# Kernel tuning notes

Measured on AMD Instinct MI355X. Metric: run time of the kernel, lower is better.

The kernel has to match this reference:

```python
import jax, jax.numpy as jnp
import numpy as np

N_NODES = 100000
N_EDGES = 1600000
NC = 32
N_MID = 8  # blocks 1..8 share structure [nc, nc//2, nc]


def setup_inputs() -> dict:
    key = jax.random.key(0)
    ks = jax.random.split(key, 12)
    x = jax.random.normal(ks[0], (N_NODES, 1), dtype=jnp.float32)
    edge_index = jax.random.randint(ks[1], (2, N_EDGES), 0, N_NODES, dtype=jnp.int32)
    s = 0.1
    # block 0: MLP [1, 16, 32]
    W1_0 = jax.random.normal(ks[2], (1, NC // 2), dtype=jnp.float32) * s
    b1_0 = jnp.zeros((NC // 2,), dtype=jnp.float32)
    W2_0 = jax.random.normal(ks[3], (NC // 2, NC), dtype=jnp.float32) * s
    b2_0 = jnp.zeros((NC,), dtype=jnp.float32)
    # blocks 1..8: MLP [32, 16, 32], stacked
    W1_mid = jax.random.normal(ks[4], (N_MID, NC, NC // 2), dtype=jnp.float32) * s
    b1_mid = jnp.zeros((N_MID, NC // 2), dtype=jnp.float32)
    W2_mid = jax.random.normal(ks[5], (N_MID, NC // 2, NC), dtype=jnp.float32) * s
    b2_mid = jnp.zeros((N_MID, NC), dtype=jnp.float32)
    # block 9: Linear(32, 1, bias=False)
    W_last = jax.random.normal(ks[6], (NC, 1), dtype=jnp.float32) * s
    return {
        "x": x, "edge_index": edge_index,
        "W1_0": W1_0, "b1_0": b1_0, "W2_0": W2_0, "b2_0": b2_0,
        "W1_mid": W1_mid, "b1_mid": b1_mid, "W2_mid": W2_mid, "b2_mid": b2_mid,
        "W_last": W_last,
    }


def _aggregate(h, src, dst):
    # GINConv sum aggregation: scatter-add messages x[src] into dst, eps=0.
    msg = h[src]  # [E, C]
    agg = jax.ops.segment_sum(msg, dst, num_segments=N_NODES)
    return h + agg  # (1+eps)*x + sum_j x_j, eps=0


def reference(x, edge_index, W1_0, b1_0, W2_0, b2_0,
              W1_mid, b1_mid, W2_mid, b2_mid, W_last):
    src = edge_index[0]
    dst = edge_index[1]
    # block 0: MLP([1,16,32]) -> Linear, SELU, (Dropout p=0 = id), Linear; no residual (1 != 32)
    h = _aggregate(x, src, dst)
    h = jax.nn.selu(h @ W1_0 + b1_0) @ W2_0 + b2_0
    # blocks 1..8: MLP([32,16,32]) with residual
    for i in range(N_MID):
        o = h
        h = _aggregate(h, src, dst)
        h = jax.nn.selu(h @ W1_mid[i] + b1_mid[i]) @ W2_mid[i] + b2_mid[i]
        h = h + o
    # block 9: Linear(32, 1, bias=False); no residual (32 != 1)
    h = _aggregate(h, src, dst)
    return h @ W_last
```

## Files before the change

### kernel.cpp

```cpp
#include <hip/hip_runtime.h>
#include <hip/hip_fp16.h>


typedef unsigned int uint_t;

#define NBLK 256
#define NBMAX 400

struct alignas(16) H2x4 { __half2 x, y, z, w; };

static __device__ __forceinline__ float selu_f(float x) {
    const float scale = 1.0507009873554805f;
    const float alpha = 1.6732632423543772f;
    return x > 0.f ? scale * x : scale * alpha * (__expf(x) - 1.f);
}

static __device__ __forceinline__ int pb0(int v) {
    return __builtin_amdgcn_mov_dpp(v, 0xA0, 0xf, 0xf, true);
}
static __device__ __forceinline__ int pb1(int v) {
    return __builtin_amdgcn_mov_dpp(v, 0xF5, 0xf, 0xf, true);
}
static __device__ __forceinline__ float pswap(float x) {
    return __int_as_float(__builtin_amdgcn_mov_dpp(__float_as_int(x), 0xB1, 0xf, 0xf, true));
}

static __device__ __forceinline__ void acc_add(__half2& a0, __half2& a1,
                                               __half2& a2, __half2& a3, H2x4 v) {
    a0 = __hadd2(a0, v.x); a1 = __hadd2(a1, v.y);
    a2 = __hadd2(a2, v.z); a3 = __hadd2(a3, v.w);
}


__global__ void k_hist(const int* __restrict__ dst, int* __restrict__ MT,
                       int e, int nb) {
    __shared__ int hist[NBMAX];
    for (int t = threadIdx.x; t < nb; t += 256) hist[t] = 0;
    __syncthreads();
    int chunk = (e + NBLK - 1) / NBLK;
    int lo = blockIdx.x * chunk, hi = min(e, lo + chunk);
    for (int i = lo + threadIdx.x; i < hi; i += 256)
        atomicAdd(&hist[dst[i] >> 8], 1);
    __syncthreads();
    for (int t = threadIdx.x; t < nb; t += 256)
        MT[t * NBLK + blockIdx.x] = hist[t];
}

__global__ void k_cscan(int* __restrict__ MT, int* __restrict__ tot, int nb) {
    int k = blockIdx.x;
    int lane = threadIdx.x;
    int carry = 0;
    #pragma unroll
    for (int r = 0; r < NBLK; r += 64) {
        int v = MT[k * NBLK + r + lane];
        int inc = v;
        #pragma unroll
        for (int d = 1; d < 64; d <<= 1) {
            int w = __shfl_up(inc, d, 64);
            if (lane >= d) inc += w;
        }
        MT[k * NBLK + r + lane] = carry + inc - v;
        carry += __shfl(inc, 63, 64);
    }
    if (lane == 0) tot[k] = carry;
}

__global__ void k_bscan(const int* __restrict__ tot, int* __restrict__ base,
                        int* __restrict__ rp, int nb, int e, int n) {
    __shared__ int s[512];
    int t = threadIdx.x;
    int v = (t < nb) ? tot[t] : 0;
    s[t] = v;
    __syncthreads();
    #pragma unroll
    for (int d = 1; d < 512; d <<= 1) {
        int w = (t >= d) ? s[t - d] : 0;
        __syncthreads();
        s[t] += w;
        __syncthreads();
    }
    if (t < nb) base[t] = s[t] - v;
    if (t == nb - 1) base[nb] = s[t];
    if (t == 0) rp[n] = e;
}

__global__ void k_scatter(const int* __restrict__ src, const int* __restrict__ dst,
                          const int* __restrict__ MT, const int* __restrict__ base,
                          uint_t* __restrict__ pairs, int e, int nb) {
    __shared__ int cur[NBMAX];
    for (int t = threadIdx.x; t < nb; t += 256)
        cur[t] = base[t] + MT[t * NBLK + blockIdx.x];
    __syncthreads();
    int chunk = (e + NBLK - 1) / NBLK;
    int lo = blockIdx.x * chunk, hi = min(e, lo + chunk);
    for (int i = lo + threadIdx.x; i < hi; i += 256) {
        int d = dst[i];
        int pos = atomicAdd(&cur[d >> 8], 1);
        pairs[pos] = (uint_t)src[i] | ((uint_t)(d & 255) << 24);
    }
}

__global__ void k_build(const uint_t* __restrict__ pairs, const int* __restrict__ base,
                        int* __restrict__ rp, int* __restrict__ esrc, int n) {
    int k = blockIdx.x;
    int bb = base[k], be = base[k + 1];
    __shared__ int cnt[256], cur[256], stmp[256];
    int t = threadIdx.x;
    cnt[t] = 0;
    __syncthreads();
    for (int i = bb + t; i < be; i += 256)
        atomicAdd(&cnt[pairs[i] >> 24], 1);
    __syncthreads();
    int v = cnt[t];
    stmp[t] = v;
    __syncthreads();
    #pragma unroll
    for (int d = 1; d < 256; d <<= 1) {
        int w = (t >= d) ? stmp[t - d] : 0;
        __syncthreads();
        stmp[t] += w;
        __syncthreads();
    }
    int excl = stmp[t] - v;
    int nd = k * 256 + t;
    if (nd < n) rp[nd] = bb + excl;
    cur[t] = bb + excl;
    __syncthreads();
    for (int i = bb + t; i < be; i += 256) {
        uint_t p = pairs[i];
        int pos = atomicAdd(&cur[p >> 24], 1);
        esrc[pos] = (int)(p & 0xFFFFFFu);
    }
}


__global__ void k_b0g(const float* __restrict__ x, const int* __restrict__ rp,
                      const int* __restrict__ esrc,
                      const float* __restrict__ W1, const float* __restrict__ b1,
                      const float* __restrict__ W2, const float* __restrict__ b2,
                      const float* __restrict__ W1next,
                      __half2* __restrict__ hout, __half2* __restrict__ gout, int n) {
    __shared__ float sW1[16], sb1[16], sW2[512], sb2[32], sWn[512];
    if (threadIdx.x < 16) { sW1[threadIdx.x] = W1[threadIdx.x]; sb1[threadIdx.x] = b1[threadIdx.x]; }
    for (int t = threadIdx.x; t < 512; t += 256) { sW2[t] = W2[t]; sWn[t] = W1next[t]; }
    if (threadIdx.x < 32) sb2[threadIdx.x] = b2[threadIdx.x];
    __syncthreads();
    int i = blockIdx.x * blockDim.x + threadIdx.x;
    if (i >= n) return;
    float a = x[i];
    int b = rp[i], en = rp[i + 1];
    int j = b;
    for (; j + 4 <= en; j += 4) {
        int s0 = esrc[j], s1 = esrc[j + 1], s2 = esrc[j + 2], s3 = esrc[j + 3];
        float x0 = x[s0], x1 = x[s1], x2 = x[s2], x3 = x[s3];
        a += (x0 + x1) + (x2 + x3);
    }
    for (; j < en; ++j) a += x[esrc[j]];
    float u[16];
    #pragma unroll
    for (int k = 0; k < 16; ++k) u[k] = selu_f(fmaf(a, sW1[k], sb1[k]));
    float row[32];
    #pragma unroll
    for (int jj = 0; jj < 32; ++jj) {
        float acc = sb2[jj];
        #pragma unroll
        for (int k = 0; k < 16; ++k) acc = fmaf(u[k], sW2[k * 32 + jj], acc);
        row[jj] = acc;
    }
    H2x4* op = (H2x4*)hout + (size_t)i * 4;
    #pragma unroll
    for (int q = 0; q < 4; ++q) {
        H2x4 vv;
        vv.x = __floats2half2_rn(row[q * 8 + 0], row[q * 8 + 1]);
        vv.y = __floats2half2_rn(row[q * 8 + 2], row[q * 8 + 3]);
        vv.z = __floats2half2_rn(row[q * 8 + 4], row[q * 8 + 5]);
        vv.w = __floats2half2_rn(row[q * 8 + 6], row[q * 8 + 7]);
        op[q] = vv;
    }
    float g[16];
    #pragma unroll
    for (int k = 0; k < 16; ++k) g[k] = 0.f;
    #pragma unroll
    for (int c = 0; c < 32; ++c) {
        float vc = row[c];
        #pragma unroll
        for (int k = 0; k < 16; ++k) g[k] = fmaf(vc, sWn[c * 16 + k], g[k]);
    }
    H2x4* gp = (H2x4*)gout + (size_t)i * 2;
    #pragma unroll
    for (int q = 0; q < 2; ++q) {
        H2x4 vv;
        vv.x = __floats2half2_rn(g[q * 8 + 0], g[q * 8 + 1]);
        vv.y = __floats2half2_rn(g[q * 8 + 2], g[q * 8 + 3]);
        vv.z = __floats2half2_rn(g[q * 8 + 4], g[q * 8 + 5]);
        vv.w = __floats2half2_rn(g[q * 8 + 6], g[q * 8 + 7]);
        gp[q] = vv;
    }
}

template<int MODE>
__global__ __launch_bounds__(256, 4) void k_gmid(
    const __half2* __restrict__ gin, const __half2* __restrict__ hin,
    const int* __restrict__ rp, const int* __restrict__ esrc,
    const float* __restrict__ W2, const float* __restrict__ b1,
    const float* __restrict__ b2, const float* __restrict__ Wnext,
    __half2* __restrict__ hout, __half2* __restrict__ gout,
    float* __restrict__ zout, int n) {
    __shared__ float sW2[512], sb1[16], sb2[32];
    __shared__ float sWn[512];
    for (int t = threadIdx.x; t < 512; t += 256) sW2[t] = W2[t];
    if (MODE == 0) {
        for (int t = threadIdx.x; t < 512; t += 256) sWn[t] = Wnext[t];
    } else {
        if (threadIdx.x < 32) sWn[threadIdx.x] = Wnext[threadIdx.x];
    }
    if (threadIdx.x < 16) sb1[threadIdx.x] = b1[threadIdx.x];
    else if (threadIdx.x < 48) sb2[threadIdx.x - 16] = b2[threadIdx.x - 16];
    __syncthreads();

    const int lane2 = threadIdx.x & 1;
    const int node = blockIdx.x * 128 + (threadIdx.x >> 1);
    if (node >= n) return;

    const H2x4* grows = (const H2x4*)gin;
    H2x4 a = grows[(size_t)node * 2 + lane2];
    __half2 a0 = a.x, a1 = a.y, a2 = a.z, a3 = a.w;

    int b = rp[node];
    int deg = rp[node + 1] - b;
    int j0 = 0;
    for (; j0 + 8 <= deg; j0 += 8) {
        int e0 = esrc[b + j0 + lane2];
        int e1 = esrc[b + j0 + 2 + lane2];
        int e2 = esrc[b + j0 + 4 + lane2];
        int e3 = esrc[b + j0 + 6 + lane2];
        int s0 = pb0(e0), s1 = pb1(e0), s2 = pb0(e1), s3 = pb1(e1);
        int s4 = pb0(e2), s5 = pb1(e2), s6 = pb0(e3), s7 = pb1(e3);
        H2x4 v0 = grows[(size_t)s0 * 2 + lane2];
        H2x4 v1 = grows[(size_t)s1 * 2 + lane2];
        H2x4 v2 = grows[(size_t)s2 * 2 + lane2];
        H2x4 v3 = grows[(size_t)s3 * 2 + lane2];
        H2x4 v4 = grows[(size_t)s4 * 2 + lane2];
        H2x4 v5 = grows[(size_t)s5 * 2 + lane2];
        H2x4 v6 = grows[(size_t)s6 * 2 + lane2];
        H2x4 v7 = grows[(size_t)s7 * 2 + lane2];
        acc_add(a0, a1, a2, a3, v0);
        acc_add(a0, a1, a2, a3, v1);
        acc_add(a0, a1, a2, a3, v2);
        acc_add(a0, a1, a2, a3, v3);
        acc_add(a0, a1, a2, a3, v4);
        acc_add(a0, a1, a2, a3, v5);
        acc_add(a0, a1, a2, a3, v6);
        acc_add(a0, a1, a2, a3, v7);
    }
    for (; j0 < deg; ++j0) {
        int s = esrc[b + j0];
        H2x4 v = grows[(size_t)s * 2 + lane2];
        acc_add(a0, a1, a2, a3, v);
    }

    float2 f0 = __half22float2(a0), f1 = __half22float2(a1),
           f2 = __half22float2(a2), f3 = __half22float2(a3);
    float u[8] = {f0.x, f0.y, f1.x, f1.y, f2.x, f2.y, f3.x, f3.y};
    const int kb = lane2 * 8;
    #pragma unroll
    for (int q = 0; q < 8; ++q) u[q] = selu_f(u[q] + sb1[kb + q]);

    float ua[16];
    #pragma unroll
    for (int q = 0; q < 8; ++q) {
        float uo = pswap(u[q]);
        ua[q]     = lane2 ? uo   : u[q];
        ua[8 + q] = lane2 ? u[q] : uo;
    }

    const H2x4* hrows = (const H2x4*)hin;
    H2x4 h0 = hrows[(size_t)node * 4 + lane2 * 2];
    H2x4 h1 = hrows[(size_t)node * 4 + lane2 * 2 + 1];
    float hv[16];
    {
        float2 g0 = __half22float2(h0.x), g1 = __half22float2(h0.y),
               g2 = __half22float2(h0.z), g3 = __half22float2(h0.w);
        float2 g4 = __half22float2(h1.x), g5 = __half22float2(h1.y),
               g6 = __half22float2(h1.z), g7 = __half22float2(h1.w);
        hv[0] = g0.x; hv[1] = g0.y; hv[2] = g1.x; hv[3] = g1.y;
        hv[4] = g2.x; hv[5] = g2.y; hv[6] = g3.x; hv[7] = g3.y;
        hv[8] = g4.x; hv[9] = g4.y; hv[10] = g5.x; hv[11] = g5.y;
        hv[12] = g6.x; hv[13] = g6.y; hv[14] = g7.x; hv[15] = g7.y;
    }

    const int jb = lane2 * 16;
    float o[16];
    #pragma unroll
    for (int q = 0; q < 16; ++q) {
        float oo = sb2[jb + q];
        #pragma unroll
        for (int k = 0; k < 16; ++k) oo = fmaf(ua[k], sW2[k * 32 + jb + q], oo);
        o[q] = oo + hv[q];
    }

    if (MODE == 0) {
        H2x4 o0, o1;
        o0.x = __floats2half2_rn(o[0], o[1]);   o0.y = __floats2half2_rn(o[2], o[3]);
        o0.z = __floats2half2_rn(o[4], o[5]);   o0.w = __floats2half2_rn(o[6], o[7]);
        o1.x = __floats2half2_rn(o[8], o[9]);   o1.y = __floats2half2_rn(o[10], o[11]);
        o1.z = __floats2half2_rn(o[12], o[13]); o1.w = __floats2half2_rn(o[14], o[15]);
        ((H2x4*)hout)[(size_t)node * 4 + lane2 * 2]     = o0;
        ((H2x4*)hout)[(size_t)node * 4 + lane2 * 2 + 1] = o1;
        float gp[16];
        #pragma unroll
        for (int k = 0; k < 16; ++k) gp[k] = 0.f;
        #pragma unroll
        for (int q = 0; q < 16; ++q) {
            float vc = o[q];
            #pragma unroll
            for (int k = 0; k < 16; ++k)
                gp[k] = fmaf(vc, sWn[(jb + q) * 16 + k], gp[k]);
        }
        #pragma unroll
        for (int k = 0; k < 16; ++k) gp[k] += pswap(gp[k]);
        H2x4 gv;
        gv.x = __floats2half2_rn(gp[kb + 0], gp[kb + 1]);
        gv.y = __floats2half2_rn(gp[kb + 2], gp[kb + 3]);
        gv.z = __floats2half2_rn(gp[kb + 4], gp[kb + 5]);
        gv.w = __floats2half2_rn(gp[kb + 6], gp[kb + 7]);
        ((H2x4*)gout)[(size_t)node * 2 + lane2] = gv;
    } else {
        float zp = 0.f;
        #pragma unroll
        for (int q = 0; q < 16; ++q) zp = fmaf(o[q], sWn[jb + q], zp);
        zp += pswap(zp);
        if (lane2 == 0) zout[node] = zp;
    }
}

__global__ void k_gz(const float* __restrict__ z, const int* __restrict__ rp,
                     const int* __restrict__ esrc, float* __restrict__ out, int n) {
    int i = blockIdx.x * blockDim.x + threadIdx.x;
    if (i >= n) return;
    float acc = z[i];
    int b = rp[i], en = rp[i + 1];
    int j = b;
    for (; j + 4 <= en; j += 4) {
        int s0 = esrc[j], s1 = esrc[j + 1], s2 = esrc[j + 2], s3 = esrc[j + 3];
        float z0 = z[s0], z1 = z[s1], z2 = z[s2], z3 = z[s3];
        acc += (z0 + z1) + (z2 + z3);
    }
    for (; j < en; ++j) acc += z[esrc[j]];
    out[i] = acc;
}


extern "C" void kernel_launch(void* const* d_in, const int* in_sizes, int n_in,
                              void* d_out, int out_size, void* d_ws, size_t ws_size,
                              hipStream_t stream) {
    const float* x    = (const float*)d_in[0];
    const int*   ei   = (const int*)d_in[1];
    const float* W1_0 = (const float*)d_in[2];
    const float* b1_0 = (const float*)d_in[3];
    const float* W2_0 = (const float*)d_in[4];
    const float* b2_0 = (const float*)d_in[5];
    const float* W1m  = (const float*)d_in[6];
    const float* b1m  = (const float*)d_in[7];
    const float* W2m  = (const float*)d_in[8];
    const float* b2m  = (const float*)d_in[9];
    const float* Wl   = (const float*)d_in[10];

    const int n = in_sizes[0];
    const int e = in_sizes[1] / 2;
    const int* src  = ei;
    const int* dstp = ei + e;
    const int nb = (n + 255) >> 8;

    char* ws = (char*)d_ws;
    size_t off = 0;
    auto alloc = [&](size_t bytes) -> char* {
        char* p = ws + off;
        off += (bytes + 255) & ~size_t(255);
        return p;
    };
    __half2* hP   = (__half2*)alloc((size_t)n * 32 * 2);
    __half2* hQ   = (__half2*)alloc((size_t)n * 32 * 2);
    __half2* gA   = (__half2*)alloc((size_t)n * 16 * 2);
    __half2* gB   = (__half2*)alloc((size_t)n * 16 * 2);
    float*   z    = (float*)alloc((size_t)n * 4);
    int*     rp   = (int*)alloc((size_t)(n + 1) * 4);
    int*     esrc = (int*)alloc((size_t)e * 4);
    uint_t*  pairs= (uint_t*)alloc((size_t)e * 4);
    int*     MT   = (int*)alloc((size_t)NBMAX * NBLK * 4);
    int*     base = (int*)alloc((size_t)(NBMAX + 1) * 4);
    int*     tot  = (int*)alloc((size_t)NBMAX * 4);
    (void)ws_size;

    const int B = 256;
    const int gN = (n + B - 1) / B;
    const int gG = (n + 127) / 128;

    k_hist<<<NBLK, B, 0, stream>>>(dstp, MT, e, nb);
    k_cscan<<<nb, 64, 0, stream>>>(MT, tot, nb);
    k_bscan<<<1, 512, 0, stream>>>(tot, base, rp, nb, e, n);
    k_scatter<<<NBLK, B, 0, stream>>>(src, dstp, MT, base, pairs, e, nb);
    k_build<<<nb, B, 0, stream>>>(pairs, base, rp, esrc, n);

    k_b0g<<<gN, B, 0, stream>>>(x, rp, esrc, W1_0, b1_0, W2_0, b2_0,
                                W1m , hP, gA, n);

    __half2* A = hP;  __half2* Bf = hQ;
    __half2* gin = gA; __half2* gnx = gB;
    for (int i = 0; i < 8; ++i) {
        if (i < 7) {
            k_gmid<0><<<gG, B, 0, stream>>>(gin, A, rp, esrc, W2m + i * 512,
                                            b1m + i * 16, b2m + i * 32,
                                            W1m + (i + 1) * 512,
                                            Bf, gnx, nullptr, n);
        } else {
            k_gmid<1><<<gG, B, 0, stream>>>(gin, A, rp, esrc, W2m + i * 512,
                                            b1m + i * 16, b2m + i * 32,
                                            Wl, Bf, nullptr, z, n);
        }
        __half2* t = A; A = Bf; Bf = t;
        __half2* tg = gin; gin = gnx; gnx = tg;
    }

    k_gz<<<gN, B, 0, stream>>>(z, rp, esrc, (float*)d_out, n);
}
```

Measured before the change: 267.7 us.

## Sort nodes by in-degree and process gather kernels in degree order

Builds a degree histogram during CSR construction, then scans it and scatters node ids into a permutation grouped by in-degree. All gather kernels (block 0, the mid blocks and the final z gather) now walk nodes through this permutation, so lanes in a wavefront have similar loop trip counts. This targets divergence from varied degrees, at the cost of two extra small kernels, a memset and one indirection per node, which makes the row reads and writes of hidden state non-contiguous. It also swaps size_t index arithmetic for 32-bit int arithmetic.

```diff
diff --git a/kernel.cpp b/kernel.cpp
--- a/kernel.cpp
+++ b/kernel.cpp
@@ -101,17 +101,21 @@
 }
 
 __global__ void k_build(const uint_t* __restrict__ pairs, const int* __restrict__ base,
-                        int* __restrict__ rp, int* __restrict__ esrc, int n) {
+                        int* __restrict__ rp, int* __restrict__ esrc,
+                        int* __restrict__ DH2, int n) {
     int k = blockIdx.x;
     int bb = base[k], be = base[k + 1];
-    __shared__ int cnt[256], cur[256], stmp[256];
+    __shared__ int cnt[256], cur[256], stmp[256], dh[64];
     int t = threadIdx.x;
     cnt[t] = 0;
+    if (t < 64) dh[t] = 0;
     __syncthreads();
     for (int i = bb + t; i < be; i += 256)
         atomicAdd(&cnt[pairs[i] >> 24], 1);
     __syncthreads();
     int v = cnt[t];
+    int nd = k * 256 + t;
+    if (nd < n) atomicAdd(&dh[min(v, 63)], 1);
     stmp[t] = v;
     __syncthreads();
     #pragma unroll
@@ -122,9 +126,9 @@
         __syncthreads();
     }
     int excl = stmp[t] - v;
-    int nd = k * 256 + t;
     if (nd < n) rp[nd] = bb + excl;
     cur[t] = bb + excl;
+    if (t < 64 && dh[t] > 0) atomicAdd(&DH2[t], dh[t]);
     __syncthreads();
     for (int i = bb + t; i < be; i += 256) {
         uint_t p = pairs[i];
@@ -133,9 +137,45 @@
     }
 }
 
+__global__ void k_dbase(const int* __restrict__ DH2, int* __restrict__ gcur) {
+    int lane = threadIdx.x;
+    int v = DH2[lane];
+    int inc = v;
+    #pragma unroll
+    for (int d = 1; d < 64; d <<= 1) {
+        int w = __shfl_up(inc, d, 64);
+        if (lane >= d) inc += w;
+    }
+    gcur[lane] = inc - v;
+}
+
+__global__ void k_dscatter(const int* __restrict__ rp, int* __restrict__ gcur,
+                           int* __restrict__ perm, int n) {
+    __shared__ int hist[64], bbase[64], cur2[64];
+    int t = threadIdx.x;
+    if (t < 64) hist[t] = 0;
+    __syncthreads();
+    int nd = blockIdx.x * 256 + t;
+    int bucket = 0;
+    if (nd < n) {
+        int deg = rp[nd + 1] - rp[nd];
+        bucket = min(deg, 63);
+        atomicAdd(&hist[bucket], 1);
+    }
+    __syncthreads();
+    if (t < 64 && hist[t] > 0) bbase[t] = atomicAdd(&gcur[t], hist[t]);
+    __syncthreads();
+    if (t < 64) cur2[t] = (hist[t] > 0) ? bbase[t] : 0;
+    __syncthreads();
+    if (nd < n) {
+        int pos = atomicAdd(&cur2[bucket], 1);
+        perm[pos] = nd;
+    }
+}
+
 
 __global__ void k_b0g(const float* __restrict__ x, const int* __restrict__ rp,
-                      const int* __restrict__ esrc,
+                      const int* __restrict__ esrc, const int* __restrict__ perm,
                       const float* __restrict__ W1, const float* __restrict__ b1,
                       const float* __restrict__ W2, const float* __restrict__ b2,
                       const float* __restrict__ W1next,
@@ -145,8 +185,9 @@
     for (int t = threadIdx.x; t < 512; t += 256) { sW2[t] = W2[t]; sWn[t] = W1next[t]; }
     if (threadIdx.x < 32) sb2[threadIdx.x] = b2[threadIdx.x];
     __syncthreads();
-    int i = blockIdx.x * blockDim.x + threadIdx.x;
-    if (i >= n) return;
+    int idx = blockIdx.x * blockDim.x + threadIdx.x;
+    if (idx >= n) return;
+    const int i = perm[idx];
     float a = x[i];
     int b = rp[i], en = rp[i + 1];
     int j = b;
@@ -167,7 +208,7 @@
         for (int k = 0; k < 16; ++k) acc = fmaf(u[k], sW2[k * 32 + jj], acc);
         row[jj] = acc;
     }
-    H2x4* op = (H2x4*)hout + (size_t)i * 4;
+    H2x4* op = (H2x4*)hout + i * 4;
     #pragma unroll
     for (int q = 0; q < 4; ++q) {
         H2x4 vv;
@@ -186,7 +227,7 @@
         #pragma unroll
         for (int k = 0; k < 16; ++k) g[k] = fmaf(vc, sWn[c * 16 + k], g[k]);
     }
-    H2x4* gp = (H2x4*)gout + (size_t)i * 2;
+    H2x4* gp = (H2x4*)gout + i * 2;
     #pragma unroll
     for (int q = 0; q < 2; ++q) {
         H2x4 vv;
@@ -202,6 +243,7 @@
 __global__ __launch_bounds__(256, 4) void k_gmid(
     const __half2* __restrict__ gin, const __half2* __restrict__ hin,
     const int* __restrict__ rp, const int* __restrict__ esrc,
+    const int* __restrict__ perm,
     const float* __restrict__ W2, const float* __restrict__ b1,
     const float* __restrict__ b2, const float* __restrict__ Wnext,
     __half2* __restrict__ hout, __half2* __restrict__ gout,
@@ -219,11 +261,12 @@
     __syncthreads();
 
     const int lane2 = threadIdx.x & 1;
-    const int node = blockIdx.x * 128 + (threadIdx.x >> 1);
-    if (node >= n) return;
+    const int idx = blockIdx.x * 128 + (threadIdx.x >> 1);
+    if (idx >= n) return;
+    const int node = perm[idx];
 
     const H2x4* grows = (const H2x4*)gin;
-    H2x4 a = grows[(size_t)node * 2 + lane2];
+    H2x4 a = grows[node * 2 + lane2];
     __half2 a0 = a.x, a1 = a.y, a2 = a.z, a3 = a.w;
 
     int b = rp[node];
@@ -236,14 +279,14 @@
         int e3 = esrc[b + j0 + 6 + lane2];
         int s0 = pb0(e0), s1 = pb1(e0), s2 = pb0(e1), s3 = pb1(e1);
         int s4 = pb0(e2), s5 = pb1(e2), s6 = pb0(e3), s7 = pb1(e3);
-        H2x4 v0 = grows[(size_t)s0 * 2 + lane2];
-        H2x4 v1 = grows[(size_t)s1 * 2 + lane2];
-        H2x4 v2 = grows[(size_t)s2 * 2 + lane2];
-        H2x4 v3 = grows[(size_t)s3 * 2 + lane2];
-        H2x4 v4 = grows[(size_t)s4 * 2 + lane2];
-        H2x4 v5 = grows[(size_t)s5 * 2 + lane2];
-        H2x4 v6 = grows[(size_t)s6 * 2 + lane2];
-        H2x4 v7 = grows[(size_t)s7 * 2 + lane2];
+        H2x4 v0 = grows[s0 * 2 + lane2];
+        H2x4 v1 = grows[s1 * 2 + lane2];
+        H2x4 v2 = grows[s2 * 2 + lane2];
+        H2x4 v3 = grows[s3 * 2 + lane2];
+        H2x4 v4 = grows[s4 * 2 + lane2];
+        H2x4 v5 = grows[s5 * 2 + lane2];
+        H2x4 v6 = grows[s6 * 2 + lane2];
+        H2x4 v7 = grows[s7 * 2 + lane2];
         acc_add(a0, a1, a2, a3, v0);
         acc_add(a0, a1, a2, a3, v1);
         acc_add(a0, a1, a2, a3, v2);
@@ -255,7 +298,7 @@
     }
     for (; j0 < deg; ++j0) {
         int s = esrc[b + j0];
-        H2x4 v = grows[(size_t)s * 2 + lane2];
+        H2x4 v = grows[s * 2 + lane2];
         acc_add(a0, a1, a2, a3, v);
     }
 
@@ -275,8 +318,8 @@
     }
 
     const H2x4* hrows = (const H2x4*)hin;
-    H2x4 h0 = hrows[(size_t)node * 4 + lane2 * 2];
-    H2x4 h1 = hrows[(size_t)node * 4 + lane2 * 2 + 1];
+    H2x4 h0 = hrows[node * 4 + lane2 * 2];
+    H2x4 h1 = hrows[node * 4 + lane2 * 2 + 1];
     float hv[16];
     {
         float2 g0 = __half22float2(h0.x), g1 = __half22float2(h0.y),
@@ -305,8 +348,8 @@
         o0.z = __floats2half2_rn(o[4], o[5]);   o0.w = __floats2half2_rn(o[6], o[7]);
         o1.x = __floats2half2_rn(o[8], o[9]);   o1.y = __floats2half2_rn(o[10], o[11]);
         o1.z = __floats2half2_rn(o[12], o[13]); o1.w = __floats2half2_rn(o[14], o[15]);
-        ((H2x4*)hout)[(size_t)node * 4 + lane2 * 2]     = o0;
-        ((H2x4*)hout)[(size_t)node * 4 + lane2 * 2 + 1] = o1;
+        ((H2x4*)hout)[node * 4 + lane2 * 2]     = o0;
+        ((H2x4*)hout)[node * 4 + lane2 * 2 + 1] = o1;
         float gp[16];
         #pragma unroll
         for (int k = 0; k < 16; ++k) gp[k] = 0.f;
@@ -324,7 +367,7 @@
         gv.y = __floats2half2_rn(gp[kb + 2], gp[kb + 3]);
         gv.z = __floats2half2_rn(gp[kb + 4], gp[kb + 5]);
         gv.w = __floats2half2_rn(gp[kb + 6], gp[kb + 7]);
-        ((H2x4*)gout)[(size_t)node * 2 + lane2] = gv;
+        ((H2x4*)gout)[node * 2 + lane2] = gv;
     } else {
         float zp = 0.f;
         #pragma unroll
@@ -335,9 +378,11 @@
 }
 
 __global__ void k_gz(const float* __restrict__ z, const int* __restrict__ rp,
-                     const int* __restrict__ esrc, float* __restrict__ out, int n) {
-    int i = blockIdx.x * blockDim.x + threadIdx.x;
-    if (i >= n) return;
+                     const int* __restrict__ esrc, const int* __restrict__ perm,
+                     float* __restrict__ out, int n) {
+    int idx = blockIdx.x * blockDim.x + threadIdx.x;
+    if (idx >= n) return;
+    const int i = perm[idx];
     float acc = z[i];
     int b = rp[i], en = rp[i + 1];
     int j = b;
@@ -390,37 +435,44 @@
     int*     MT   = (int*)alloc((size_t)NBMAX * NBLK * 4);
     int*     base = (int*)alloc((size_t)(NBMAX + 1) * 4);
     int*     tot  = (int*)alloc((size_t)NBMAX * 4);
+    int*     perm = (int*)alloc((size_t)n * 4);
+    int*     DH2  = (int*)alloc(64 * 4);
+    int*     gcur = (int*)alloc(64 * 4);
     (void)ws_size;
 
     const int B = 256;
     const int gN = (n + B - 1) / B;
     const int gG = (n + 127) / 128;
 
+    hipMemsetAsync(DH2, 0, 64 * 4, stream);
     k_hist<<<NBLK, B, 0, stream>>>(dstp, MT, e, nb);
     k_cscan<<<nb, 64, 0, stream>>>(MT, tot, nb);
     k_bscan<<<1, 512, 0, stream>>>(tot, base, rp, nb, e, n);
     k_scatter<<<NBLK, B, 0, stream>>>(src, dstp, MT, base, pairs, e, nb);
-    k_build<<<nb, B, 0, stream>>>(pairs, base, rp, esrc, n);
-
-    k_b0g<<<gN, B, 0, stream>>>(x, rp, esrc, W1_0, b1_0, W2_0, b2_0,
+    k_build<<<nb, B, 0, stream>>>(pairs, base, rp, esrc, DH2, n);
+    k_dbase<<<1, 64, 0, stream>>>(DH2, gcur);
+    k_dscatter<<<nb, B, 0, stream>>>(rp, gcur, perm, n);
+
+    k_b0g<<<gN, B, 0, stream>>>(x, rp, esrc, perm, W1_0, b1_0, W2_0, b2_0,
                                 W1m , hP, gA, n);
 
     __half2* A = hP;  __half2* Bf = hQ;
     __half2* gin = gA; __half2* gnx = gB;
     for (int i = 0; i < 8; ++i) {
         if (i < 7) {
-            k_gmid<0><<<gG, B, 0, stream>>>(gin, A, rp, esrc, W2m + i * 512,
-                                            b1m + i * 16, b2m + i * 32,
-                                            W1m + (i + 1) * 512,
+            k_gmid<0><<<gG, B, 0, stream>>>(gin, A, rp, esrc, perm,
+                                            W2m + i * 512, b1m + i * 16,
+                                            b2m + i * 32, W1m + (i + 1) * 512,
                                             Bf, gnx, nullptr, n);
         } else {
-            k_gmid<1><<<gG, B, 0, stream>>>(gin, A, rp, esrc, W2m + i * 512,
-                                            b1m + i * 16, b2m + i * 32,
-                                            Wl, Bf, nullptr, z, n);
+            k_gmid<1><<<gG, B, 0, stream>>>(gin, A, rp, esrc, perm,
+                                            W2m + i * 512, b1m + i * 16,
+                                            b2m + i * 32, Wl,
+                                            Bf, nullptr, z, n);
         }
         __half2* t = A; A = Bf; Bf = t;
         __half2* tg = gin; gin = gnx; gnx = tg;
     }
 
-    k_gz<<<gN, B, 0, stream>>>(z, rp, esrc, (float*)d_out, n);
-}
+    k_gz<<<gN, B, 0, stream>>>(z, rp, esrc, perm, (float*)d_out, n);
+}
```

Result: slower. 334.9 us (+25.1%).

## Use four lanes per node in gather-MLP kernels and two lanes in scalar gathers

Applied to the files above, without the earlier changes.

Each node in the middle GIN layers is now handled by four lanes instead of two. Two lane pairs gather alternate 8-edge chunks, padding with a zeroed dummy row at index n, and their sums are combined through DPP row swaps. The dense W2/Wnext products are split so each lane computes 8 output columns using float4 LDS reads. The first-layer kernel and the final scalar aggregation now split each node's edge list across two lanes. The aim is more memory-level parallelism and lower per-thread latency on the irregular gathers, at the cost of extra masked loads, cross-lane reductions and two small memsets.

```diff
diff --git a/kernel.cpp b/kernel.cpp
--- a/kernel.cpp
+++ b/kernel.cpp
@@ -8,6 +8,7 @@
 #define NBMAX 400
 
 struct alignas(16) H2x4 { __half2 x, y, z, w; };
+struct alignas(8)  H2x2 { __half2 x, y; };
 
 static __device__ __forceinline__ float selu_f(float x) {
     const float scale = 1.0507009873554805f;
@@ -23,6 +24,15 @@
 }
 static __device__ __forceinline__ float pswap(float x) {
     return __int_as_float(__builtin_amdgcn_mov_dpp(__float_as_int(x), 0xB1, 0xf, 0xf, true));
+}
+static __device__ __forceinline__ float qx2f(float x) {
+    return __int_as_float(__builtin_amdgcn_mov_dpp(__float_as_int(x), 0x4E, 0xf, 0xf, true));
+}
+static __device__ __forceinline__ __half2 h2qx2(__half2 v) {
+    int i; __builtin_memcpy(&i, &v, 4);
+    i = __builtin_amdgcn_mov_dpp(i, 0x4E, 0xf, 0xf, true);
+    __half2 r; __builtin_memcpy(&r, &i, 4);
+    return r;
 }
 
 static __device__ __forceinline__ void acc_add(__half2& a0, __half2& a1,
@@ -134,68 +144,100 @@
 }
 
 
-__global__ void k_b0g(const float* __restrict__ x, const int* __restrict__ rp,
-                      const int* __restrict__ esrc,
-                      const float* __restrict__ W1, const float* __restrict__ b1,
-                      const float* __restrict__ W2, const float* __restrict__ b2,
-                      const float* __restrict__ W1next,
-                      __half2* __restrict__ hout, __half2* __restrict__ gout, int n) {
-    __shared__ float sW1[16], sb1[16], sW2[512], sb2[32], sWn[512];
-    if (threadIdx.x < 16) { sW1[threadIdx.x] = W1[threadIdx.x]; sb1[threadIdx.x] = b1[threadIdx.x]; }
+__global__ __launch_bounds__(256) void k_b0g(
+    const float* __restrict__ x, const int* __restrict__ rp,
+    const int* __restrict__ esrc,
+    const float* __restrict__ W1, const float* __restrict__ b1,
+    const float* __restrict__ W2, const float* __restrict__ b2,
+    const float* __restrict__ W1next,
+    __half2* __restrict__ hout, __half2* __restrict__ gout, int n) {
+    __shared__ __align__(16) float sW1[16], sb1v[16], sW2[512], sb2v[32], sWn[512];
+    if (threadIdx.x < 16) { sW1[threadIdx.x] = W1[threadIdx.x]; sb1v[threadIdx.x] = b1[threadIdx.x]; }
     for (int t = threadIdx.x; t < 512; t += 256) { sW2[t] = W2[t]; sWn[t] = W1next[t]; }
-    if (threadIdx.x < 32) sb2[threadIdx.x] = b2[threadIdx.x];
-    __syncthreads();
-    int i = blockIdx.x * blockDim.x + threadIdx.x;
-    if (i >= n) return;
-    float a = x[i];
-    int b = rp[i], en = rp[i + 1];
-    int j = b;
-    for (; j + 4 <= en; j += 4) {
-        int s0 = esrc[j], s1 = esrc[j + 1], s2 = esrc[j + 2], s3 = esrc[j + 3];
-        float x0 = x[s0], x1 = x[s1], x2 = x[s2], x3 = x[s3];
-        a += (x0 + x1) + (x2 + x3);
-    }
-    for (; j < en; ++j) a += x[esrc[j]];
+    if (threadIdx.x < 32) sb2v[threadIdx.x] = b2[threadIdx.x];
+    __syncthreads();
+    const int lane2 = threadIdx.x & 1;
+    const int node = blockIdx.x * 128 + (threadIdx.x >> 1);
+    if (node >= n) return;
+
+    const int b = rp[node];
+    const int deg = rp[node + 1] - b;
+    const int half = deg >> 1;
+    const int lo = lane2 ? half : 0;
+    const int hi = lane2 ? deg : half;
+    float a = lane2 ? 0.f : x[node];
+    int j = lo;
+    for (; j + 4 <= hi; j += 4) {
+        int s0 = esrc[b + j], s1 = esrc[b + j + 1],
+            s2 = esrc[b + j + 2], s3 = esrc[b + j + 3];
+        float v0 = x[s0], v1 = x[s1], v2 = x[s2], v3 = x[s3];
+        a += (v0 + v1) + (v2 + v3);
+    }
+    for (; j < hi; ++j) a += x[esrc[b + j]];
+    a += pswap(a);
+
     float u[16];
     #pragma unroll
-    for (int k = 0; k < 16; ++k) u[k] = selu_f(fmaf(a, sW1[k], sb1[k]));
-    float row[32];
-    #pragma unroll
-    for (int jj = 0; jj < 32; ++jj) {
-        float acc = sb2[jj];
-        #pragma unroll
-        for (int k = 0; k < 16; ++k) acc = fmaf(u[k], sW2[k * 32 + jj], acc);
-        row[jj] = acc;
-    }
-    H2x4* op = (H2x4*)hout + (size_t)i * 4;
-    #pragma unroll
-    for (int q = 0; q < 4; ++q) {
-        H2x4 vv;
-        vv.x = __floats2half2_rn(row[q * 8 + 0], row[q * 8 + 1]);
-        vv.y = __floats2half2_rn(row[q * 8 + 2], row[q * 8 + 3]);
-        vv.z = __floats2half2_rn(row[q * 8 + 4], row[q * 8 + 5]);
-        vv.w = __floats2half2_rn(row[q * 8 + 6], row[q * 8 + 7]);
-        op[q] = vv;
-    }
-    float g[16];
-    #pragma unroll
-    for (int k = 0; k < 16; ++k) g[k] = 0.f;
-    #pragma unroll
-    for (int c = 0; c < 32; ++c) {
-        float vc = row[c];
-        #pragma unroll
-        for (int k = 0; k < 16; ++k) g[k] = fmaf(vc, sWn[c * 16 + k], g[k]);
-    }
-    H2x4* gp = (H2x4*)gout + (size_t)i * 2;
-    #pragma unroll
-    for (int q = 0; q < 2; ++q) {
-        H2x4 vv;
-        vv.x = __floats2half2_rn(g[q * 8 + 0], g[q * 8 + 1]);
-        vv.y = __floats2half2_rn(g[q * 8 + 2], g[q * 8 + 3]);
-        vv.z = __floats2half2_rn(g[q * 8 + 4], g[q * 8 + 5]);
-        vv.w = __floats2half2_rn(g[q * 8 + 6], g[q * 8 + 7]);
-        gp[q] = vv;
-    }
+    for (int k = 0; k < 16; ++k) u[k] = selu_f(fmaf(a, sW1[k], sb1v[k]));
+
+    const int jb = lane2 * 16;
+    float row[16];
+    #pragma unroll
+    for (int q = 0; q < 16; ++q) row[q] = sb2v[jb + q];
+    #pragma unroll
+    for (int k = 0; k < 16; ++k) {
+        const float4 w0 = *(const float4*)&sW2[k * 32 + jb];
+        const float4 w1 = *(const float4*)&sW2[k * 32 + jb + 4];
+        const float4 w2 = *(const float4*)&sW2[k * 32 + jb + 8];
+        const float4 w3 = *(const float4*)&sW2[k * 32 + jb + 12];
+        float uk = u[k];
+        row[0]  = fmaf(uk, w0.x, row[0]);  row[1]  = fmaf(uk, w0.y, row[1]);
+        row[2]  = fmaf(uk, w0.z, row[2]);  row[3]  = fmaf(uk, w0.w, row[3]);
+        row[4]  = fmaf(uk, w1.x, row[4]);  row[5]  = fmaf(uk, w1.y, row[5]);
+        row[6]  = fmaf(uk, w1.z, row[6]);  row[7]  = fmaf(uk, w1.w, row[7]);
+        row[8]  = fmaf(uk, w2.x, row[8]);  row[9]  = fmaf(uk, w2.y, row[9]);
+        row[10] = fmaf(uk, w2.z, row[10]); row[11] = fmaf(uk, w2.w, row[11]);
+        row[12] = fmaf(uk, w3.x, row[12]); row[13] = fmaf(uk, w3.y, row[13]);
+        row[14] = fmaf(uk, w3.z, row[14]); row[15] = fmaf(uk, w3.w, row[15]);
+    }
+    H2x4 o0, o1;
+    o0.x = __floats2half2_rn(row[0], row[1]);   o0.y = __floats2half2_rn(row[2], row[3]);
+    o0.z = __floats2half2_rn(row[4], row[5]);   o0.w = __floats2half2_rn(row[6], row[7]);
+    o1.x = __floats2half2_rn(row[8], row[9]);   o1.y = __floats2half2_rn(row[10], row[11]);
+    o1.z = __floats2half2_rn(row[12], row[13]); o1.w = __floats2half2_rn(row[14], row[15]);
+    ((H2x4*)hout)[node * 4 + lane2 * 2]     = o0;
+    ((H2x4*)hout)[node * 4 + lane2 * 2 + 1] = o1;
+
+    float gp[16];
+    #pragma unroll
+    for (int k = 0; k < 16; ++k) gp[k] = 0.f;
+    #pragma unroll
+    for (int q = 0; q < 16; ++q) {
+        const float4 w0 = *(const float4*)&sWn[(jb + q) * 16];
+        const float4 w1 = *(const float4*)&sWn[(jb + q) * 16 + 4];
+        const float4 w2 = *(const float4*)&sWn[(jb + q) * 16 + 8];
+        const float4 w3 = *(const float4*)&sWn[(jb + q) * 16 + 12];
+        float vq = row[q];
+        gp[0]  = fmaf(vq, w0.x, gp[0]);  gp[1]  = fmaf(vq, w0.y, gp[1]);
+        gp[2]  = fmaf(vq, w0.z, gp[2]);  gp[3]  = fmaf(vq, w0.w, gp[3]);
+        gp[4]  = fmaf(vq, w1.x, gp[4]);  gp[5]  = fmaf(vq, w1.y, gp[5]);
+        gp[6]  = fmaf(vq, w1.z, gp[6]);  gp[7]  = fmaf(vq, w1.w, gp[7]);
+        gp[8]  = fmaf(vq, w2.x, gp[8]);  gp[9]  = fmaf(vq, w2.y, gp[9]);
+        gp[10] = fmaf(vq, w2.z, gp[10]); gp[11] = fmaf(vq, w2.w, gp[11]);
+        gp[12] = fmaf(vq, w3.x, gp[12]); gp[13] = fmaf(vq, w3.y, gp[13]);
+        gp[14] = fmaf(vq, w3.z, gp[14]); gp[15] = fmaf(vq, w3.w, gp[15]);
+    }
+    float r[8];
+    #pragma unroll
+    for (int i = 0; i < 8; ++i) {
+        float lo_ = gp[i]     + pswap(gp[i]);
+        float hi_ = gp[8 + i] + pswap(gp[8 + i]);
+        r[i] = lane2 ? hi_ : lo_;
+    }
+    H2x4 gv;
+    gv.x = __floats2half2_rn(r[0], r[1]); gv.y = __floats2half2_rn(r[2], r[3]);
+    gv.z = __floats2half2_rn(r[4], r[5]); gv.w = __floats2half2_rn(r[6], r[7]);
+    ((H2x4*)gout)[node * 2 + lane2] = gv;
 }
 
 template<int MODE>
@@ -206,8 +248,7 @@
     const float* __restrict__ b2, const float* __restrict__ Wnext,
     __half2* __restrict__ hout, __half2* __restrict__ gout,
     float* __restrict__ zout, int n) {
-    __shared__ float sW2[512], sb1[16], sb2[32];
-    __shared__ float sWn[512];
+    __shared__ __align__(16) float sW2[512], sb1[16], sb2[32], sWn[512];
     for (int t = threadIdx.x; t < 512; t += 256) sW2[t] = W2[t];
     if (MODE == 0) {
         for (int t = threadIdx.x; t < 512; t += 256) sWn[t] = Wnext[t];
@@ -218,32 +259,42 @@
     else if (threadIdx.x < 48) sb2[threadIdx.x - 16] = b2[threadIdx.x - 16];
     __syncthreads();
 
-    const int lane2 = threadIdx.x & 1;
-    const int node = blockIdx.x * 128 + (threadIdx.x >> 1);
+    const int lane4 = threadIdx.x & 3;
+    const int c = lane4 & 1;
+    const int p = lane4 >> 1;
+    const int node = blockIdx.x * 64 + (threadIdx.x >> 2);
     if (node >= n) return;
 
     const H2x4* grows = (const H2x4*)gin;
-    H2x4 a = grows[(size_t)node * 2 + lane2];
-    __half2 a0 = a.x, a1 = a.y, a2 = a.z, a3 = a.w;
-
-    int b = rp[node];
-    int deg = rp[node + 1] - b;
-    int j0 = 0;
-    for (; j0 + 8 <= deg; j0 += 8) {
-        int e0 = esrc[b + j0 + lane2];
-        int e1 = esrc[b + j0 + 2 + lane2];
-        int e2 = esrc[b + j0 + 4 + lane2];
-        int e3 = esrc[b + j0 + 6 + lane2];
+    H2x4 self = grows[node * 2 + c];
+    __half2 hzero = __floats2half2_rn(0.f, 0.f);
+    __half2 a0 = p ? hzero : self.x, a1 = p ? hzero : self.y,
+            a2 = p ? hzero : self.z, a3 = p ? hzero : self.w;
+
+    const int b = rp[node];
+    const int deg = rp[node + 1] - b;
+    const int ZR = n;
+    for (int j0 = 0; j0 < deg; j0 += 16) {
+        int lo = j0 + 8 * p;
+        int m = deg - lo; m = m < 0 ? 0 : (m > 8 ? 8 : m);
+        int i0 = lo + c,     i1 = lo + 2 + c, i2 = lo + 4 + c, i3 = lo + 6 + c;
+        i0 = i0 < deg ? i0 : 0; i1 = i1 < deg ? i1 : 0;
+        i2 = i2 < deg ? i2 : 0; i3 = i3 < deg ? i3 : 0;
+        int e0 = esrc[b + i0], e1 = esrc[b + i1], e2 = esrc[b + i2], e3 = esrc[b + i3];
         int s0 = pb0(e0), s1 = pb1(e0), s2 = pb0(e1), s3 = pb1(e1);
         int s4 = pb0(e2), s5 = pb1(e2), s6 = pb0(e3), s7 = pb1(e3);
-        H2x4 v0 = grows[(size_t)s0 * 2 + lane2];
-        H2x4 v1 = grows[(size_t)s1 * 2 + lane2];
-        H2x4 v2 = grows[(size_t)s2 * 2 + lane2];
-        H2x4 v3 = grows[(size_t)s3 * 2 + lane2];
-        H2x4 v4 = grows[(size_t)s4 * 2 + lane2];
-        H2x4 v5 = grows[(size_t)s5 * 2 + lane2];
-        H2x4 v6 = grows[(size_t)s6 * 2 + lane2];
-        H2x4 v7 = grows[(size_t)s7 * 2 + lane2];
+        s0 = 0 < m ? s0 : ZR; s1 = 1 < m ? s1 : ZR;
+        s2 = 2 < m ? s2 : ZR; s3 = 3 < m ? s3 : ZR;
+        s4 = 4 < m ? s4 : ZR; s5 = 5 < m ? s5 : ZR;
+        s6 = 6 < m ? s6 : ZR; s7 = 7 < m ? s7 : ZR;
+        H2x4 v0 = grows[s0 * 2 + c];
+        H2x4 v1 = grows[s1 * 2 + c];
+        H2x4 v2 = grows[s2 * 2 + c];
+        H2x4 v3 = grows[s3 * 2 + c];
+        H2x4 v4 = grows[s4 * 2 + c];
+        H2x4 v5 = grows[s5 * 2 + c];
+        H2x4 v6 = grows[s6 * 2 + c];
+        H2x4 v7 = grows[s7 * 2 + c];
         acc_add(a0, a1, a2, a3, v0);
         acc_add(a0, a1, a2, a3, v1);
         acc_add(a0, a1, a2, a3, v2);
@@ -253,16 +304,13 @@
         acc_add(a0, a1, a2, a3, v6);
         acc_add(a0, a1, a2, a3, v7);
     }
-    for (; j0 < deg; ++j0) {
-        int s = esrc[b + j0];
-        H2x4 v = grows[(size_t)s * 2 + lane2];
-        acc_add(a0, a1, a2, a3, v);
-    }
+    a0 = __hadd2(a0, h2qx2(a0)); a1 = __hadd2(a1, h2qx2(a1));
+    a2 = __hadd2(a2, h2qx2(a2)); a3 = __hadd2(a3, h2qx2(a3));
 
     float2 f0 = __half22float2(a0), f1 = __half22float2(a1),
            f2 = __half22float2(a2), f3 = __half22float2(a3);
     float u[8] = {f0.x, f0.y, f1.x, f1.y, f2.x, f2.y, f3.x, f3.y};
-    const int kb = lane2 * 8;
+    const int kb = c * 8;
     #pragma unroll
     for (int q = 0; q < 8; ++q) u[q] = selu_f(u[q] + sb1[kb + q]);
 
@@ -270,84 +318,103 @@
     #pragma unroll
     for (int q = 0; q < 8; ++q) {
         float uo = pswap(u[q]);
-        ua[q]     = lane2 ? uo   : u[q];
-        ua[8 + q] = lane2 ? u[q] : uo;
-    }
-
+        ua[q]     = c ? uo   : u[q];
+        ua[8 + q] = c ? u[q] : uo;
+    }
+
+    const int jb = lane4 * 8;
     const H2x4* hrows = (const H2x4*)hin;
-    H2x4 h0 = hrows[(size_t)node * 4 + lane2 * 2];
-    H2x4 h1 = hrows[(size_t)node * 4 + lane2 * 2 + 1];
-    float hv[16];
-    {
-        float2 g0 = __half22float2(h0.x), g1 = __half22float2(h0.y),
-               g2 = __half22float2(h0.z), g3 = __half22float2(h0.w);
-        float2 g4 = __half22float2(h1.x), g5 = __half22float2(h1.y),
-               g6 = __half22float2(h1.z), g7 = __half22float2(h1.w);
-        hv[0] = g0.x; hv[1] = g0.y; hv[2] = g1.x; hv[3] = g1.y;
-        hv[4] = g2.x; hv[5] = g2.y; hv[6] = g3.x; hv[7] = g3.y;
-        hv[8] = g4.x; hv[9] = g4.y; hv[10] = g5.x; hv[11] = g5.y;
-        hv[12] = g6.x; hv[13] = g6.y; hv[14] = g7.x; hv[15] = g7.y;
-    }
-
-    const int jb = lane2 * 16;
-    float o[16];
-    #pragma unroll
-    for (int q = 0; q < 16; ++q) {
-        float oo = sb2[jb + q];
-        #pragma unroll
-        for (int k = 0; k < 16; ++k) oo = fmaf(ua[k], sW2[k * 32 + jb + q], oo);
-        o[q] = oo + hv[q];
+    H2x4 h0 = hrows[node * 4 + lane4];
+    float2 g0 = __half22float2(h0.x), g1 = __half22float2(h0.y),
+           g2 = __half22float2(h0.z), g3 = __half22float2(h0.w);
+    float o[8] = {g0.x, g0.y, g1.x, g1.y, g2.x, g2.y, g3.x, g3.y};
+    #pragma unroll
+    for (int q = 0; q < 8; ++q) o[q] += sb2[jb + q];
+    #pragma unroll
+    for (int k = 0; k < 16; ++k) {
+        const float4 w0 = *(const float4*)&sW2[k * 32 + jb];
+        const float4 w1 = *(const float4*)&sW2[k * 32 + jb + 4];
+        float uk = ua[k];
+        o[0] = fmaf(uk, w0.x, o[0]); o[1] = fmaf(uk, w0.y, o[1]);
+        o[2] = fmaf(uk, w0.z, o[2]); o[3] = fmaf(uk, w0.w, o[3]);
+        o[4] = fmaf(uk, w1.x, o[4]); o[5] = fmaf(uk, w1.y, o[5]);
+        o[6] = fmaf(uk, w1.z, o[6]); o[7] = fmaf(uk, w1.w, o[7]);
     }
 
     if (MODE == 0) {
-        H2x4 o0, o1;
-        o0.x = __floats2half2_rn(o[0], o[1]);   o0.y = __floats2half2_rn(o[2], o[3]);
-        o0.z = __floats2half2_rn(o[4], o[5]);   o0.w = __floats2half2_rn(o[6], o[7]);
-        o1.x = __floats2half2_rn(o[8], o[9]);   o1.y = __floats2half2_rn(o[10], o[11]);
-        o1.z = __floats2half2_rn(o[12], o[13]); o1.w = __floats2half2_rn(o[14], o[15]);
-        ((H2x4*)hout)[(size_t)node * 4 + lane2 * 2]     = o0;
-        ((H2x4*)hout)[(size_t)node * 4 + lane2 * 2 + 1] = o1;
+        H2x4 ov;
+        ov.x = __floats2half2_rn(o[0], o[1]); ov.y = __floats2half2_rn(o[2], o[3]);
+        ov.z = __floats2half2_rn(o[4], o[5]); ov.w = __floats2half2_rn(o[6], o[7]);
+        ((H2x4*)hout)[node * 4 + lane4] = ov;
+
         float gp[16];
         #pragma unroll
         for (int k = 0; k < 16; ++k) gp[k] = 0.f;
         #pragma unroll
-        for (int q = 0; q < 16; ++q) {
-            float vc = o[q];
-            #pragma unroll
-            for (int k = 0; k < 16; ++k)
-                gp[k] = fmaf(vc, sWn[(jb + q) * 16 + k], gp[k]);
+        for (int q = 0; q < 8; ++q) {
+            const float4 w0 = *(const float4*)&sWn[(jb + q) * 16];
+            const float4 w1 = *(const float4*)&sWn[(jb + q) * 16 + 4];
+            const float4 w2 = *(const float4*)&sWn[(jb + q) * 16 + 8];
+            const float4 w3 = *(const float4*)&sWn[(jb + q) * 16 + 12];
+            float vq = o[q];
+            gp[0]  = fmaf(vq, w0.x, gp[0]);  gp[1]  = fmaf(vq, w0.y, gp[1]);
+            gp[2]  = fmaf(vq, w0.z, gp[2]);  gp[3]  = fmaf(vq, w0.w, gp[3]);
+            gp[4]  = fmaf(vq, w1.x, gp[4]);  gp[5]  = fmaf(vq, w1.y, gp[5]);
+            gp[6]  = fmaf(vq, w1.z, gp[6]);  gp[7]  = fmaf(vq, w1.w, gp[7]);
+            gp[8]  = fmaf(vq, w2.x, gp[8]);  gp[9]  = fmaf(vq, w2.y, gp[9]);
+            gp[10] = fmaf(vq, w2.z, gp[10]); gp[11] = fmaf(vq, w2.w, gp[11]);
+            gp[12] = fmaf(vq, w3.x, gp[12]); gp[13] = fmaf(vq, w3.y, gp[13]);
+            gp[14] = fmaf(vq, w3.z, gp[14]); gp[15] = fmaf(vq, w3.w, gp[15]);
         }
-        #pragma unroll
-        for (int k = 0; k < 16; ++k) gp[k] += pswap(gp[k]);
-        H2x4 gv;
-        gv.x = __floats2half2_rn(gp[kb + 0], gp[kb + 1]);
-        gv.y = __floats2half2_rn(gp[kb + 2], gp[kb + 3]);
-        gv.z = __floats2half2_rn(gp[kb + 4], gp[kb + 5]);
-        gv.w = __floats2half2_rn(gp[kb + 6], gp[kb + 7]);
-        ((H2x4*)gout)[(size_t)node * 2 + lane2] = gv;
+        float r[8];
+        #pragma unroll
+        for (int i = 0; i < 8; ++i) {
+            float lo_ = gp[i]     + pswap(gp[i]);
+            float hi_ = gp[8 + i] + pswap(gp[8 + i]);
+            r[i] = c ? hi_ : lo_;
+        }
+        float rr[4];
+        #pragma unroll
+        for (int i = 0; i < 4; ++i) {
+            float lo_ = r[i]     + qx2f(r[i]);
+            float hi_ = r[4 + i] + qx2f(r[4 + i]);
+            rr[i] = p ? hi_ : lo_;
+        }
+        H2x2 gv;
+        gv.x = __floats2half2_rn(rr[0], rr[1]);
+        gv.y = __floats2half2_rn(rr[2], rr[3]);
+        ((H2x2*)gout)[node * 4 + c * 2 + p] = gv;
     } else {
         float zp = 0.f;
         #pragma unroll
-        for (int q = 0; q < 16; ++q) zp = fmaf(o[q], sWn[jb + q], zp);
+        for (int q = 0; q < 8; ++q) zp = fmaf(o[q], sWn[jb + q], zp);
         zp += pswap(zp);
-        if (lane2 == 0) zout[node] = zp;
+        zp += qx2f(zp);
+        if (lane4 == 0) zout[node] = zp;
     }
 }
 
 __global__ void k_gz(const float* __restrict__ z, const int* __restrict__ rp,
                      const int* __restrict__ esrc, float* __restrict__ out, int n) {
-    int i = blockIdx.x * blockDim.x + threadIdx.x;
-    if (i >= n) return;
-    float acc = z[i];
-    int b = rp[i], en = rp[i + 1];
-    int j = b;
-    for (; j + 4 <= en; j += 4) {
-        int s0 = esrc[j], s1 = esrc[j + 1], s2 = esrc[j + 2], s3 = esrc[j + 3];
+    const int lane2 = threadIdx.x & 1;
+    const int node = blockIdx.x * 128 + (threadIdx.x >> 1);
+    if (node >= n) return;
+    const int b = rp[node];
+    const int deg = rp[node + 1] - b;
+    const int half = deg >> 1;
+    const int lo = lane2 ? half : 0;
+    const int hi = lane2 ? deg : half;
+    float acc = lane2 ? 0.f : z[node];
+    int j = lo;
+    for (; j + 4 <= hi; j += 4) {
+        int s0 = esrc[b + j], s1 = esrc[b + j + 1],
+            s2 = esrc[b + j + 2], s3 = esrc[b + j + 3];
         float z0 = z[s0], z1 = z[s1], z2 = z[s2], z3 = z[s3];
         acc += (z0 + z1) + (z2 + z3);
     }
-    for (; j < en; ++j) acc += z[esrc[j]];
-    out[i] = acc;
+    for (; j < hi; ++j) acc += z[esrc[b + j]];
+    acc += pswap(acc);
+    if (lane2 == 0) out[node] = acc;
 }
 
 
@@ -368,7 +435,7 @@
 
     const int n = in_sizes[0];
     const int e = in_sizes[1] / 2;
-    const int* src  = ei;
+    const int* srcp = ei;
     const int* dstp = ei + e;
     const int nb = (n + 255) >> 8;
 
@@ -381,8 +448,8 @@
     };
     __half2* hP   = (__half2*)alloc((size_t)n * 32 * 2);
     __half2* hQ   = (__half2*)alloc((size_t)n * 32 * 2);
-    __half2* gA   = (__half2*)alloc((size_t)n * 16 * 2);
-    __half2* gB   = (__half2*)alloc((size_t)n * 16 * 2);
+    __half2* gA   = (__half2*)alloc((size_t)(n + 1) * 16 * 2);
+    __half2* gB   = (__half2*)alloc((size_t)(n + 1) * 16 * 2);
     float*   z    = (float*)alloc((size_t)n * 4);
     int*     rp   = (int*)alloc((size_t)(n + 1) * 4);
     int*     esrc = (int*)alloc((size_t)e * 4);
@@ -394,33 +461,38 @@
 
     const int B = 256;
     const int gN = (n + B - 1) / B;
-    const int gG = (n + 127) / 128;
+    const int g2 = (n + 127) / 128;
+    const int g4 = (n + 63) / 64;
+
+    hipMemsetAsync(gA + (size_t)n * 8, 0, 32, stream);
+    hipMemsetAsync(gB + (size_t)n * 8, 0, 32, stream);
 
     k_hist<<<NBLK, B, 0, stream>>>(dstp, MT, e, nb);
     k_cscan<<<nb, 64, 0, stream>>>(MT, tot, nb);
     k_bscan<<<1, 512, 0, stream>>>(tot, base, rp, nb, e, n);
-    k_scatter<<<NBLK, B, 0, stream>>>(src, dstp, MT, base, pairs, e, nb);
+    k_scatter<<<NBLK, B, 0, stream>>>(srcp, dstp, MT, base, pairs, e, nb);
     k_build<<<nb, B, 0, stream>>>(pairs, base, rp, esrc, n);
 
-    k_b0g<<<gN, B, 0, stream>>>(x, rp, esrc, W1_0, b1_0, W2_0, b2_0,
+    k_b0g<<<g2, B, 0, stream>>>(x, rp, esrc, W1_0, b1_0, W2_0, b2_0,
                                 W1m , hP, gA, n);
 
     __half2* A = hP;  __half2* Bf = hQ;
     __half2* gin = gA; __half2* gnx = gB;
     for (int i = 0; i < 8; ++i) {
         if (i < 7) {
-            k_gmid<0><<<gG, B, 0, stream>>>(gin, A, rp, esrc, W2m + i * 512,
-                                            b1m + i * 16, b2m + i * 32,
-                                            W1m + (i + 1) * 512,
+            k_gmid<0><<<g4, B, 0, stream>>>(gin, A, rp, esrc,
+                                            W2m + i * 512, b1m + i * 16,
+                                            b2m + i * 32, W1m + (i + 1) * 512,
                                             Bf, gnx, nullptr, n);
         } else {
-            k_gmid<1><<<gG, B, 0, stream>>>(gin, A, rp, esrc, W2m + i * 512,
-                                            b1m + i * 16, b2m + i * 32,
-                                            Wl, Bf, nullptr, z, n);
+            k_gmid<1><<<g4, B, 0, stream>>>(gin, A, rp, esrc,
+                                            W2m + i * 512, b1m + i * 16,
+                                            b2m + i * 32, Wl,
+                                            Bf, nullptr, z, n);
         }
         __half2* t = A; A = Bf; Bf = t;
         __half2* tg = gin; gin = gnx; gnx = tg;
     }
 
-    k_gz<<<gN, B, 0, stream>>>(z, rp, esrc, (float*)d_out, n);
-}
+    k_gz<<<g2, B, 0, stream>>>(z, rp, esrc, (float*)d_out, n);
+}
```

New measurement: 252.1 us. 5.8% less time.
